# Performance work log

Hardware: AMD Instinct MI355X
Metric: run time of the kernel (lower is better)

## Reference

```python
import jax, jax.numpy as jnp
import numpy as np

H = W = 128  # render resolution (init height/width)
EPS = 1e-8

def _normalize(x, axis):
    return x / (jnp.linalg.norm(x, axis=axis, keepdims=True) + EPS)

def _render_one(pts, camrot, campos, proj, uv, faces):
    # pts (p,3), camrot (3,3), campos (3,), proj (3,1), uv (p,2), faces (f,3)
    pc = (pts - campos) @ camrot.T                       # camera-space verts (p,3)
    xy = pc[:, :2] * proj[:2, 0] / (pc[:, 2:3] + EPS)    # perspective projection -> NDC (p,2)
    v3d = pc[faces]                                      # (f,3,3)
    v2d = xy[faces]                                      # (f,3,2)
    n = jnp.cross(v3d[:, 1] - v3d[:, 0], v3d[:, 2] - v3d[:, 0])  # face normals (f,3)
    n1 = _normalize(n, axis=1)
    # pixel grid in NDC
    px = jnp.linspace(-1.0, 1.0, W)[None, None, :]
    py = jnp.linspace(1.0, -1.0, H)[None, :, None]
    ax, ay = v2d[:, 0, 0, None, None], v2d[:, 0, 1, None, None]
    bx, by = v2d[:, 1, 0, None, None], v2d[:, 1, 1, None, None]
    cx, cy = v2d[:, 2, 0, None, None], v2d[:, 2, 1, None, None]
    d = (by - cy) * (ax - cx) + (cx - bx) * (ay - cy)    # (f,1,1) signed 2*area
    l0 = ((by - cy) * (px - cx) + (cx - bx) * (py - cy)) / (d + EPS)
    l1 = ((cy - ay) * (px - cx) + (ax - cx) * (py - cy)) / (d + EPS)
    l2 = 1.0 - l0 - l1                                   # barycentrics (f,H,W)
    z = (l0 * v3d[:, 0, 2, None, None] + l1 * v3d[:, 1, 2, None, None]
         + l2 * v3d[:, 2, 2, None, None])                # interpolated depth (f,H,W)
    inside = (l0 >= 0) & (l1 >= 0) & (l2 >= 0) & (jnp.abs(d) > EPS) & (z > EPS)
    zm = jnp.where(inside, z, jnp.float32(1e10))
    idx = jnp.argmin(zm, axis=0)                         # nearest visible face per pixel (H,W)
    hard = jnp.any(inside, axis=0)[..., None].astype(pts.dtype)  # hardmask (H,W,1)
    take = lambda a: jnp.take_along_axis(a, idx[None], axis=0)[0]  # (H,W)
    uvsel = uv[faces][idx]                               # (H,W,3,2) per-pixel face uvs
    tc = (take(l0)[..., None] * uvsel[..., 0, :]
          + take(l1)[..., None] * uvsel[..., 1, :]
          + take(l2)[..., None] * uvsel[..., 2, :]) * hard  # imtexcoords (H,W,2)
    return tc, hard, n1

def _fragment_shader(tc, texture, mask):
    # nearest-filter texture lookup; texture (3,th,tw)
    th, tw = texture.shape[1], texture.shape[2]
    u = jnp.clip(tc[..., 0], 0.0, 1.0)
    v = jnp.clip(tc[..., 1], 0.0, 1.0)
    tx = jnp.round(u * (tw - 1)).astype(jnp.int32)
    ty = jnp.round((1.0 - v) * (th - 1)).astype(jnp.int32)
    color = texture[:, ty, tx].transpose(1, 2, 0)        # (H,W,3)
    return color * mask

def setup_inputs() -> dict:
    key = jax.random.key(0)
    ks = jax.random.split(key, 6)
    b, p, f = 3, 768, 1024
    points = jax.random.normal(ks[0], (b, p, 3), jnp.float32) * 0.3
    faces = jax.random.randint(ks[1], (f, 3), 0, p)
    camera_rot = jnp.broadcast_to(jnp.eye(3, dtype=jnp.float32), (b, 3, 3))
    camera_pos = jnp.zeros((b, 3), jnp.float32).at[:, 2].set(-3.0)  # objects in front of camera
    camera_proj = jnp.ones((3, 1), jnp.float32)
    uv = jax.random.uniform(ks[2], (b, p, 2), jnp.float32)
    texture = jax.random.uniform(ks[3], (b, 3, 512, 512), jnp.float32)
    ts = jax.random.normal(ks[4], (b, 3), jnp.float32)
    return dict(points=points, camera_rot=camera_rot, camera_pos=camera_pos,
                camera_proj=camera_proj, uv=uv, texture=texture, ts=ts, faces=faces)

def reference(points, camera_rot, camera_pos, camera_proj, uv, texture, ts, faces):
    b = points.shape[0]
    render = jax.vmap(_render_one, in_axes=(0, 0, 0, None, 0, None))
    tcs, masks, normals = render(points, camera_rot, camera_pos, camera_proj, uv, faces)
    ims = jax.vmap(_fragment_shader)(tcs, texture, masks)   # (b,H,W,3)
    probs = masks                                            # improb proxy == hardmask
    order = jnp.argsort(-ts[:, 2])                           # far -> near compositing order
    ims_s, probs_s, masks_s = ims[order], probs[order], masks[order]
    imrender, improb, fg = ims_s[0], probs_s[0], masks_s[0]
    for i in range(1, b):                                    # fixed small layer count
        m = masks_s[i] > 0.5
        imrender = jnp.where(m, ims_s[i], imrender)
        improb = jnp.where(m, probs_s[i], improb)
        fg = jnp.where(m, masks_s[i], fg)
    return imrender[None], improb[None], normals, fg[None]
```

## Files before the change

### kernel.cpp

```cpp
#include <hip/hip_runtime.h>
#include <math.h>

#define B_ 3
#define P_ 768
#define F_ 1024
#define H_ 128
#define W_ 128
#define HW_ (H_*W_)
#define EPS_ 1e-8f

#define OFF_PROB   49152
#define OFF_NORM   65536
#define OFF_FG     74752


__global__ __launch_bounds__(256) void raster_fwd(
    const float* __restrict__ points,
    const float* __restrict__ camrot,
    const float* __restrict__ campos,
    const float* __restrict__ proj,
    const int*   __restrict__ faces,
    float4* __restrict__ faceA,
    float4* __restrict__ faceB,
    float4* __restrict__ faceC,
    float2* __restrict__ faceD,
    const float* __restrict__ uv,
    unsigned long long* __restrict__ packed,
    float*  __restrict__ normals_out)
{
#pragma clang fp contract(off)
    int wid  = blockIdx.x * 4 + (threadIdx.x >> 6);
    int sub  = blockIdx.y;
    int lane = threadIdx.x & 63;
    int b = wid / F_;
    int f = wid - b * F_;

    const float* R = camrot + b * 9;
    float cpx = campos[b*3+0], cpy = campos[b*3+1], cpz = campos[b*3+2];
    float pj0 = proj[0], pj1 = proj[1];

    int idx3[3];
    float pcx[3], pcy[3], pcz[3], sx[3], sy[3];
    for (int v = 0; v < 3; ++v) {
        int vi = faces[f*3 + v];
        idx3[v] = vi;
        const float* P = points + (b*P_ + vi) * 3;
        float vx = P[0] - cpx;
        float vy = P[1] - cpy;
        float vz = P[2] - cpz;
        float qx = (vx*R[0] + vy*R[1]) + vz*R[2];
        float qy = (vx*R[3] + vy*R[4]) + vz*R[5];
        float qz = (vx*R[6] + vy*R[7]) + vz*R[8];
        pcx[v] = qx; pcy[v] = qy; pcz[v] = qz;
        float dz = qz + EPS_;
        sx[v] = (qx * pj0) / dz;
        sy[v] = (qy * pj1) / dz;
    }

    float ax = sx[0], ay = sy[0];
    float bx = sx[1], by = sy[1];
    float cx = sx[2], cy = sy[2];

    float e0x = by - cy;
    float e0y = cx - bx;
    float e1x = cy - ay;
    float e1y = ax - cx;
    float d = e0x*(ax - cx) + e0y*(ay - cy);
    float denom = d + EPS_;
    bool valid = fabsf(d) > EPS_;
    float z0 = pcz[0], z1 = pcz[1], z2 = pcz[2];

    if (lane == 0 && sub == 0) {
        faceA[wid] = make_float4(e0x, e0y, e1x, e1y);
        faceB[wid] = make_float4(cx, cy, denom, valid ? 1.0f : 0.0f);
        const float* uvb = uv + b * P_ * 2;
        faceC[wid] = make_float4(uvb[idx3[0]*2+0], uvb[idx3[0]*2+1],
                                 uvb[idx3[1]*2+0], uvb[idx3[1]*2+1]);
        faceD[wid] = make_float2(uvb[idx3[2]*2+0], uvb[idx3[2]*2+1]);

        float ux = pcx[1]-pcx[0], uy = pcy[1]-pcy[0], uz = pcz[1]-pcz[0];
        float wx = pcx[2]-pcx[0], wy = pcy[2]-pcy[0], wz = pcz[2]-pcz[0];
        float nx = fmaf(uy, wz, -(uz*wy));
        float ny = fmaf(uz, wx, -(ux*wz));
        float nz = fmaf(ux, wy, -(uy*wx));
        float nn = sqrtf((nx*nx + ny*ny) + nz*nz) + 1e-8f;
        normals_out[wid*3+0] = nx / nn;
        normals_out[wid*3+1] = ny / nn;
        normals_out[wid*3+2] = nz / nn;
    }

    if (!valid) return;

    float gx0 = (ax + 1.0f) * 63.5f;
    float gx1 = (bx + 1.0f) * 63.5f;
    float gx2 = (cx + 1.0f) * 63.5f;
    float gy0 = (1.0f - ay) * 63.5f;
    float gy1 = (1.0f - by) * 63.5f;
    float gy2 = (1.0f - cy) * 63.5f;
    int xlo = max(0,   (int)ceilf (fminf(fminf(gx0,gx1),gx2) - 1.0f));
    int xhi = min(127, (int)floorf(fmaxf(fmaxf(gx0,gx1),gx2) + 1.0f));
    int ylo = max(0,   (int)ceilf (fminf(fminf(gy0,gy1),gy2) - 1.0f));
    int yhi = min(127, (int)floorf(fmaxf(fmaxf(gy0,gy1),gy2) + 1.0f));
    int wX = xhi - xlo + 1;
    int wY = yhi - ylo + 1;
    if (wX <= 0 || wY <= 0) return;
    int N = wX * wY;

    int i0 = sub * 64 + lane;
    if (i0 >= N) return;
    int q = 128 / wX;
    int r = 128 - q * wX;
    int yy = i0 / wX;
    int xx = i0 - yy * wX;

    const double STEP = 2.0 / 127.0;
    unsigned long long* cells = packed + b * HW_;

    for (int i = i0; i < N; i += 128) {
        int X = xlo + xx;
        int Y = ylo + yy;
        float px = (float)(-1.0 + (double)X * STEP);
        float py = (float)( 1.0 - (double)Y * STEP);
        float dx = px - cx;
        float dy = py - cy;
        float n0 = e0x*dx + e0y*dy;
        float n1 = e1x*dx + e1y*dy;
        float l0 = n0 / denom;
        float l1 = n1 / denom;
        float l2 = 1.0f - l0 - l1;
        float zz = (l0*z0 + l1*z1) + l2*z2;
        if (l0 >= 0.0f && l1 >= 0.0f && l2 >= 0.0f && zz > EPS_) {
            unsigned long long pk =
                ((unsigned long long)__float_as_uint(zz) << 32) | (unsigned)f;
            atomicMin(&cells[Y * W_ + X], pk);
        }
        xx += r; yy += q;
        if (xx >= wX) { xx -= wX; yy += 1; }
    }
}

__global__ __launch_bounds__(128) void shade_composite(
    const float4* __restrict__ faceA,
    const float4* __restrict__ faceB,
    const float4* __restrict__ faceC,
    const float2* __restrict__ faceD,
    const float*  __restrict__ tex,
    const float*  __restrict__ ts,
    const unsigned long long* __restrict__ packed,
    float* __restrict__ out)
{
#pragma clang fp contract(off)
    int pix = blockIdx.x * 128 + threadIdx.x;
    int y = pix >> 7;
    int x = pix & (W_ - 1);

    const double STEP = 2.0 / 127.0;
    float px = (float)(-1.0 + (double)x * STEP);
    float py = (float)( 1.0 - (double)y * STEP);

    const unsigned MISS_BITS = __float_as_uint(1e10f);

    unsigned long long pks[B_];
    for (int b = 0; b < B_; ++b) pks[b] = packed[b * HW_ + pix];

    float m[B_]; int fi[B_];
    float4 A[B_], Bv[B_], Cv[B_]; float2 Dv[B_];
    for (int b = 0; b < B_; ++b) {
        bool hard = (unsigned)(pks[b] >> 32) < MISS_BITS;
        m[b]  = hard ? 1.0f : 0.0f;
        fi[b] = hard ? (int)(unsigned)pks[b] : 0;
        A[b]  = faceA[b * F_ + fi[b]];
        Bv[b] = faceB[b * F_ + fi[b]];
        Cv[b] = faceC[b * F_ + fi[b]];
        Dv[b] = faceD[b * F_ + fi[b]];
    }

    int txi[B_], tyi[B_];
    for (int b = 0; b < B_; ++b) {
        float dx = px - Bv[b].x;
        float dy = py - Bv[b].y;
        float n0 = A[b].x*dx + A[b].y*dy;
        float n1 = A[b].z*dx + A[b].w*dy;
        float l0 = n0 / Bv[b].z;
        float l1 = n1 / Bv[b].z;
        float l2 = 1.0f - l0 - l1;
        float tu = (l0*Cv[b].x + l1*Cv[b].z) + l2*Dv[b].x;
        float tv = (l0*Cv[b].y + l1*Cv[b].w) + l2*Dv[b].y;
        float uc = fminf(fmaxf(tu, 0.0f), 1.0f);
        float vc = fminf(fmaxf(tv, 0.0f), 1.0f);
        txi[b] = (int)rintf(uc * 511.0f);
        tyi[b] = (int)rintf((1.0f - vc) * 511.0f);
    }

    float rr[B_], gg[B_], bb_[B_];
    for (int b = 0; b < B_; ++b) {
        const float* tb = tex + b * 3 * 512 * 512;
        int o = tyi[b]*512 + txi[b];
        rr[b]  = tb[0*262144 + o] * m[b];
        gg[b]  = tb[1*262144 + o] * m[b];
        bb_[b] = tb[2*262144 + o] * m[b];
    }

    float k0 = ts[0*3+2], k1 = ts[1*3+2], k2 = ts[2*3+2];
    int o0 = 0, o1 = 1, o2 = 2;
    if (k1 > k0) { int ti=o0; o0=o1; o1=ti; float tf=k0; k0=k1; k1=tf; }
    if (k2 > k1) { int ti=o1; o1=o2; o2=ti; float tf=k1; k1=k2; k2=tf; }
    if (k1 > k0) { int ti=o0; o0=o1; o1=ti; float tf=k0; k0=k1; k1=tf; }

    float sr = rr[o0], sg = gg[o0], sb = bb_[o0], sm = m[o0];
    if (m[o1] > 0.5f) { sr = rr[o1]; sg = gg[o1]; sb = bb_[o1]; sm = m[o1]; }
    if (m[o2] > 0.5f) { sr = rr[o2]; sg = gg[o2]; sb = bb_[o2]; sm = m[o2]; }

    out[pix*3+0] = sr;
    out[pix*3+1] = sg;
    out[pix*3+2] = sb;
    out[OFF_PROB + pix] = sm;
    out[OFF_FG   + pix] = sm;
}

extern "C" void kernel_launch(void* const* d_in, const int* in_sizes, int n_in,
                              void* d_out, int out_size, void* d_ws, size_t ws_size,
                              hipStream_t stream) {
    const float* points = (const float*)d_in[0];
    const float* camrot = (const float*)d_in[1];
    const float* campos = (const float*)d_in[2];
    const float* proj   = (const float*)d_in[3];
    const float* uv     = (const float*)d_in[4];
    const float* tex    = (const float*)d_in[5];
    const float* ts     = (const float*)d_in[6];
    const int*   faces  = (const int*)d_in[7];
    float* out = (float*)d_out;

    char* ws = (char*)d_ws;
    float4* faceA = (float4*)(ws);
    float4* faceB = (float4*)(ws + 49152);
    float4* faceC = (float4*)(ws + 98304);
    float2* faceD = (float2*)(ws + 147456);
    unsigned long long* packed = (unsigned long long*)(ws + 172032);

    hipMemsetAsync(packed, 0xFF, (size_t)B_ * HW_ * 8, stream);

    raster_fwd<<<dim3(B_*F_/4, 2), dim3(256), 0, stream>>>(
        points, camrot, campos, proj, faces, faceA, faceB, faceC, faceD, uv,
        packed, out + OFF_NORM);
    shade_composite<<<dim3(HW_/128), dim3(128), 0, stream>>>(
        faceA, faceB, faceC, faceD, tex, ts, packed, out);
}
```

Before: 88.51 us.

## Fuse memset, raster and shade into one cooperative kernel with grid syncs

```diff
diff --git a/kernel.cpp b/kernel.cpp
--- a/kernel.cpp
+++ b/kernel.cpp
@@ -1,5 +1,8 @@
 #include <hip/hip_runtime.h>
+#include <hip/hip_cooperative_groups.h>
 #include <math.h>
+
+namespace cg = cooperative_groups;
 
 #define B_ 3
 #define P_ 768
@@ -8,32 +11,38 @@
 #define W_ 128
 #define HW_ (H_*W_)
 #define EPS_ 1e-8f
+#define NBLK_ 768
 
 #define OFF_PROB   49152
 #define OFF_NORM   65536
 #define OFF_FG     74752
 
 
-__global__ __launch_bounds__(256) void raster_fwd(
+__global__ __launch_bounds__(256) void render_fused(
     const float* __restrict__ points,
     const float* __restrict__ camrot,
     const float* __restrict__ campos,
     const float* __restrict__ proj,
     const int*   __restrict__ faces,
+    const float* __restrict__ uv,
+    const float* __restrict__ tex,
+    const float* __restrict__ ts,
     float4* __restrict__ faceA,
     float4* __restrict__ faceB,
     float4* __restrict__ faceC,
     float2* __restrict__ faceD,
-    const float* __restrict__ uv,
     unsigned long long* __restrict__ packed,
-    float*  __restrict__ normals_out)
+    float* __restrict__ out)
 {
 #pragma clang fp contract(off)
-    int wid  = blockIdx.x * 4 + (threadIdx.x >> 6);
-    int sub  = blockIdx.y;
-    int lane = threadIdx.x & 63;
-    int b = wid / F_;
-    int f = wid - b * F_;
+    cg::grid_group grid = cg::this_grid();
+    int tg   = blockIdx.x * 256 + threadIdx.x;
+    int wid  = tg >> 6;
+    int lane = tg & 63;
+    int b = wid >> 10;
+    int f = wid & (F_ - 1);
+
+    if (tg < B_ * HW_) packed[tg] = 0xFFFFFFFFFFFFFFFFull;
 
     const float* R = camrot + b * 9;
     float cpx = campos[b*3+0], cpy = campos[b*3+1], cpz = campos[b*3+2];
@@ -70,7 +79,7 @@
     bool valid = fabsf(d) > EPS_;
     float z0 = pcz[0], z1 = pcz[1], z2 = pcz[2];
 
-    if (lane == 0 && sub == 0) {
+    if (lane == 0) {
         faceA[wid] = make_float4(e0x, e0y, e1x, e1y);
         faceB[wid] = make_float4(cx, cy, denom, valid ? 1.0f : 0.0f);
         const float* uvb = uv + b * P_ * 2;
@@ -84,138 +93,131 @@
         float ny = fmaf(uz, wx, -(ux*wz));
         float nz = fmaf(ux, wy, -(uy*wx));
         float nn = sqrtf((nx*nx + ny*ny) + nz*nz) + 1e-8f;
-        normals_out[wid*3+0] = nx / nn;
-        normals_out[wid*3+1] = ny / nn;
-        normals_out[wid*3+2] = nz / nn;
-    }
-
-    if (!valid) return;
-
-    float gx0 = (ax + 1.0f) * 63.5f;
-    float gx1 = (bx + 1.0f) * 63.5f;
-    float gx2 = (cx + 1.0f) * 63.5f;
-    float gy0 = (1.0f - ay) * 63.5f;
-    float gy1 = (1.0f - by) * 63.5f;
-    float gy2 = (1.0f - cy) * 63.5f;
-    int xlo = max(0,   (int)ceilf (fminf(fminf(gx0,gx1),gx2) - 1.0f));
-    int xhi = min(127, (int)floorf(fmaxf(fmaxf(gx0,gx1),gx2) + 1.0f));
-    int ylo = max(0,   (int)ceilf (fminf(fminf(gy0,gy1),gy2) - 1.0f));
-    int yhi = min(127, (int)floorf(fmaxf(fmaxf(gy0,gy1),gy2) + 1.0f));
-    int wX = xhi - xlo + 1;
-    int wY = yhi - ylo + 1;
-    if (wX <= 0 || wY <= 0) return;
-    int N = wX * wY;
-
-    int i0 = sub * 64 + lane;
-    if (i0 >= N) return;
-    int q = 128 / wX;
-    int r = 128 - q * wX;
-    int yy = i0 / wX;
-    int xx = i0 - yy * wX;
-
-    const double STEP = 2.0 / 127.0;
-    unsigned long long* cells = packed + b * HW_;
-
-    for (int i = i0; i < N; i += 128) {
-        int X = xlo + xx;
-        int Y = ylo + yy;
-        float px = (float)(-1.0 + (double)X * STEP);
-        float py = (float)( 1.0 - (double)Y * STEP);
-        float dx = px - cx;
-        float dy = py - cy;
-        float n0 = e0x*dx + e0y*dy;
-        float n1 = e1x*dx + e1y*dy;
-        float l0 = n0 / denom;
-        float l1 = n1 / denom;
-        float l2 = 1.0f - l0 - l1;
-        float zz = (l0*z0 + l1*z1) + l2*z2;
-        if (l0 >= 0.0f && l1 >= 0.0f && l2 >= 0.0f && zz > EPS_) {
-            unsigned long long pk =
-                ((unsigned long long)__float_as_uint(zz) << 32) | (unsigned)f;
-            atomicMin(&cells[Y * W_ + X], pk);
-        }
-        xx += r; yy += q;
-        if (xx >= wX) { xx -= wX; yy += 1; }
-    }
-}
-
-__global__ __launch_bounds__(128) void shade_composite(
-    const float4* __restrict__ faceA,
-    const float4* __restrict__ faceB,
-    const float4* __restrict__ faceC,
-    const float2* __restrict__ faceD,
-    const float*  __restrict__ tex,
-    const float*  __restrict__ ts,
-    const unsigned long long* __restrict__ packed,
-    float* __restrict__ out)
-{
-#pragma clang fp contract(off)
-    int pix = blockIdx.x * 128 + threadIdx.x;
-    int y = pix >> 7;
-    int x = pix & (W_ - 1);
-
-    const double STEP = 2.0 / 127.0;
-    float px = (float)(-1.0 + (double)x * STEP);
-    float py = (float)( 1.0 - (double)y * STEP);
-
-    const unsigned MISS_BITS = __float_as_uint(1e10f);
-
-    unsigned long long pks[B_];
-    for (int b = 0; b < B_; ++b) pks[b] = packed[b * HW_ + pix];
-
-    float m[B_]; int fi[B_];
-    float4 A[B_], Bv[B_], Cv[B_]; float2 Dv[B_];
-    for (int b = 0; b < B_; ++b) {
-        bool hard = (unsigned)(pks[b] >> 32) < MISS_BITS;
-        m[b]  = hard ? 1.0f : 0.0f;
-        fi[b] = hard ? (int)(unsigned)pks[b] : 0;
-        A[b]  = faceA[b * F_ + fi[b]];
-        Bv[b] = faceB[b * F_ + fi[b]];
-        Cv[b] = faceC[b * F_ + fi[b]];
-        Dv[b] = faceD[b * F_ + fi[b]];
-    }
-
-    int txi[B_], tyi[B_];
-    for (int b = 0; b < B_; ++b) {
-        float dx = px - Bv[b].x;
-        float dy = py - Bv[b].y;
-        float n0 = A[b].x*dx + A[b].y*dy;
-        float n1 = A[b].z*dx + A[b].w*dy;
-        float l0 = n0 / Bv[b].z;
-        float l1 = n1 / Bv[b].z;
-        float l2 = 1.0f - l0 - l1;
-        float tu = (l0*Cv[b].x + l1*Cv[b].z) + l2*Dv[b].x;
-        float tv = (l0*Cv[b].y + l1*Cv[b].w) + l2*Dv[b].y;
-        float uc = fminf(fmaxf(tu, 0.0f), 1.0f);
-        float vc = fminf(fmaxf(tv, 0.0f), 1.0f);
-        txi[b] = (int)rintf(uc * 511.0f);
-        tyi[b] = (int)rintf((1.0f - vc) * 511.0f);
-    }
-
-    float rr[B_], gg[B_], bb_[B_];
-    for (int b = 0; b < B_; ++b) {
-        const float* tb = tex + b * 3 * 512 * 512;
-        int o = tyi[b]*512 + txi[b];
-        rr[b]  = tb[0*262144 + o] * m[b];
-        gg[b]  = tb[1*262144 + o] * m[b];
-        bb_[b] = tb[2*262144 + o] * m[b];
-    }
-
-    float k0 = ts[0*3+2], k1 = ts[1*3+2], k2 = ts[2*3+2];
-    int o0 = 0, o1 = 1, o2 = 2;
-    if (k1 > k0) { int ti=o0; o0=o1; o1=ti; float tf=k0; k0=k1; k1=tf; }
-    if (k2 > k1) { int ti=o1; o1=o2; o2=ti; float tf=k1; k1=k2; k2=tf; }
-    if (k1 > k0) { int ti=o0; o0=o1; o1=ti; float tf=k0; k0=k1; k1=tf; }
-
-    float sr = rr[o0], sg = gg[o0], sb = bb_[o0], sm = m[o0];
-    if (m[o1] > 0.5f) { sr = rr[o1]; sg = gg[o1]; sb = bb_[o1]; sm = m[o1]; }
-    if (m[o2] > 0.5f) { sr = rr[o2]; sg = gg[o2]; sb = bb_[o2]; sm = m[o2]; }
-
-    out[pix*3+0] = sr;
-    out[pix*3+1] = sg;
-    out[pix*3+2] = sb;
-    out[OFF_PROB + pix] = sm;
-    out[OFF_FG   + pix] = sm;
+        float* no = out + OFF_NORM + wid*3;
+        no[0] = nx / nn;
+        no[1] = ny / nn;
+        no[2] = nz / nn;
+    }
+
+    grid.sync();
+
+    if (valid) {
+        float gx0 = (ax + 1.0f) * 63.5f;
+        float gx1 = (bx + 1.0f) * 63.5f;
+        float gx2 = (cx + 1.0f) * 63.5f;
+        float gy0 = (1.0f - ay) * 63.5f;
+        float gy1 = (1.0f - by) * 63.5f;
+        float gy2 = (1.0f - cy) * 63.5f;
+        int xlo = max(0,   (int)ceilf (fminf(fminf(gx0,gx1),gx2) - 1.0f));
+        int xhi = min(127, (int)floorf(fmaxf(fmaxf(gx0,gx1),gx2) + 1.0f));
+        int ylo = max(0,   (int)ceilf (fminf(fminf(gy0,gy1),gy2) - 1.0f));
+        int yhi = min(127, (int)floorf(fmaxf(fmaxf(gy0,gy1),gy2) + 1.0f));
+        int wX = xhi - xlo + 1;
+        int wY = yhi - ylo + 1;
+        if (wX > 0 && wY > 0) {
+            int N = wX * wY;
+            int q64 = 64 / wX;
+            int r64 = 64 - q64 * wX;
+            int yy = lane / wX;
+            int xx = lane - yy * wX;
+
+            const double STEP = 2.0 / 127.0;
+            unsigned long long* cells = packed + b * HW_;
+
+            for (int i = lane; i < N; i += 64) {
+                int X = xlo + xx;
+                int Y = ylo + yy;
+                float px = (float)(-1.0 + (double)X * STEP);
+                float py = (float)( 1.0 - (double)Y * STEP);
+                float dx = px - cx;
+                float dy = py - cy;
+                float n0 = e0x*dx + e0y*dy;
+                float n1 = e1x*dx + e1y*dy;
+                float l0 = n0 / denom;
+                float l1 = n1 / denom;
+                float l2 = 1.0f - l0 - l1;
+                float zz = (l0*z0 + l1*z1) + l2*z2;
+                if (l0 >= 0.0f && l1 >= 0.0f && l2 >= 0.0f && zz > EPS_) {
+                    unsigned long long pk =
+                        ((unsigned long long)__float_as_uint(zz) << 32) | (unsigned)f;
+                    atomicMin(&cells[Y * W_ + X], pk);
+                }
+                xx += r64; yy += q64;
+                if (xx >= wX) { xx -= wX; yy += 1; }
+            }
+        }
+    }
+
+    grid.sync();
+
+    if (tg < HW_) {
+        int pix = tg;
+        int y = pix >> 7;
+        int x = pix & (W_ - 1);
+
+        const double STEP = 2.0 / 127.0;
+        float px = (float)(-1.0 + (double)x * STEP);
+        float py = (float)( 1.0 - (double)y * STEP);
+
+        const unsigned MISS_BITS = __float_as_uint(1e10f);
+
+        unsigned long long pks[B_];
+        for (int bb = 0; bb < B_; ++bb) pks[bb] = packed[bb * HW_ + pix];
+
+        float m[B_]; int fi[B_];
+        float4 A[B_], Bv[B_], Cv[B_]; float2 Dv[B_];
+        for (int bb = 0; bb < B_; ++bb) {
+            bool hard = (unsigned)(pks[bb] >> 32) < MISS_BITS;
+            m[bb]  = hard ? 1.0f : 0.0f;
+            fi[bb] = hard ? (int)(unsigned)pks[bb] : 0;
+            A[bb]  = faceA[bb * F_ + fi[bb]];
+            Bv[bb] = faceB[bb * F_ + fi[bb]];
+            Cv[bb] = faceC[bb * F_ + fi[bb]];
+            Dv[bb] = faceD[bb * F_ + fi[bb]];
+        }
+
+        int txi[B_], tyi[B_];
+        for (int bb = 0; bb < B_; ++bb) {
+            float dx = px - Bv[bb].x;
+            float dy = py - Bv[bb].y;
+            float n0 = A[bb].x*dx + A[bb].y*dy;
+            float n1 = A[bb].z*dx + A[bb].w*dy;
+            float l0 = n0 / Bv[bb].z;
+            float l1 = n1 / Bv[bb].z;
+            float l2 = 1.0f - l0 - l1;
+            float tu = (l0*Cv[bb].x + l1*Cv[bb].z) + l2*Dv[bb].x;
+            float tv = (l0*Cv[bb].y + l1*Cv[bb].w) + l2*Dv[bb].y;
+            float uc = fminf(fmaxf(tu, 0.0f), 1.0f);
+            float vc = fminf(fmaxf(tv, 0.0f), 1.0f);
+            txi[bb] = (int)rintf(uc * 511.0f);
+            tyi[bb] = (int)rintf((1.0f - vc) * 511.0f);
+        }
+
+        float rr[B_], gg[B_], bl[B_];
+        for (int bb = 0; bb < B_; ++bb) {
+            const float* tb = tex + bb * 3 * 262144;
+            int o = tyi[bb]*512 + txi[bb];
+            rr[bb] = tb[0*262144 + o] * m[bb];
+            gg[bb] = tb[1*262144 + o] * m[bb];
+            bl[bb] = tb[2*262144 + o] * m[bb];
+        }
+
+        float k0 = ts[0*3+2], k1 = ts[1*3+2], k2 = ts[2*3+2];
+        int o0 = 0, o1 = 1, o2 = 2;
+        if (k1 > k0) { int ti=o0; o0=o1; o1=ti; float tf=k0; k0=k1; k1=tf; }
+        if (k2 > k1) { int ti=o1; o1=o2; o2=ti; float tf=k1; k1=k2; k2=tf; }
+        if (k1 > k0) { int ti=o0; o0=o1; o1=ti; float tf=k0; k0=k1; k1=tf; }
+
+        float sr = rr[o0], sg = gg[o0], sb = bl[o0], sm = m[o0];
+        if (m[o1] > 0.5f) { sr = rr[o1]; sg = gg[o1]; sb = bl[o1]; sm = m[o1]; }
+        if (m[o2] > 0.5f) { sr = rr[o2]; sg = gg[o2]; sb = bl[o2]; sm = m[o2]; }
+
+        out[pix*3+0] = sr;
+        out[pix*3+1] = sg;
+        out[pix*3+2] = sb;
+        out[OFF_PROB + pix] = sm;
+        out[OFF_FG   + pix] = sm;
+    }
 }
 
 extern "C" void kernel_launch(void* const* d_in, const int* in_sizes, int n_in,
@@ -238,11 +240,12 @@
     float2* faceD = (float2*)(ws + 147456);
     unsigned long long* packed = (unsigned long long*)(ws + 172032);
 
-    hipMemsetAsync(packed, 0xFF, (size_t)B_ * HW_ * 8, stream);
-
-    raster_fwd<<<dim3(B_*F_/4, 2), dim3(256), 0, stream>>>(
-        points, camrot, campos, proj, faces, faceA, faceB, faceC, faceD, uv,
-        packed, out + OFF_NORM);
-    shade_composite<<<dim3(HW_/128), dim3(128), 0, stream>>>(
-        faceA, faceB, faceC, faceD, tex, ts, packed, out);
+    void* args[] = {
+        (void*)&points, (void*)&camrot, (void*)&campos, (void*)&proj,
+        (void*)&faces,  (void*)&uv,     (void*)&tex,    (void*)&ts,
+        (void*)&faceA,  (void*)&faceB,  (void*)&faceC,  (void*)&faceD,
+        (void*)&packed, (void*)&out
+    };
+    hipLaunchCooperativeKernel((const void*)render_fused,
+                               dim3(NBLK_), dim3(256), args, 0, stream);
 }
```

After: 226.1 us. 2.55x slower.
